# Optimization experiments

Measured on AMD Instinct MI355X. Metric: run time of the kernel, lower is better.

## Reference

```python
import jax, jax.numpy as jnp
from jax import lax
import numpy as np

EPS = 1e-5

def setup_inputs() -> dict:
    key = jax.random.key(0)
    k1, k2, k3, k4 = jax.random.split(key, 4)
    B, in_c, out_c, k, z_dim, H, W = 16, 128, 256, 3, 256, 64, 64
    fan_in = in_c * k * k
    x = jax.random.normal(k1, (B, in_c, H, W), dtype=jnp.float32)
    z = jax.random.normal(k2, (B, z_dim), dtype=jnp.float32)
    base_weight = jax.random.normal(k3, (out_c, in_c, k, k), dtype=jnp.float32) * np.sqrt(2.0 / fan_in)
    head_w = jax.random.normal(k4, (out_c * in_c * k * k, z_dim), dtype=jnp.float32) * np.sqrt(1.0 / z_dim)
    return {"x": x, "z": z, "base_weight": base_weight, "head_w": head_w}

def reference(x, z, base_weight, head_w):
    # x: [B, in_c, H, W]; z: [B, z_dim]; base_weight: [out_c, in_c, k, k]; head_w: [out_c*in_c*k*k, z_dim]
    B = x.shape[0]
    out_c, in_c, k, _ = base_weight.shape
    fan_in = in_c * k * k
    hyper_weight = 1.0

    # delta_w = Linear(z) -> [B, out_c, in_c, k, k]
    delta_w = jnp.einsum('bz,oz->bo', z, head_w).reshape(B, out_c, in_c, k, k)
    # standardize over (in_c, k, k) per (sample, out-channel)
    mu = jnp.mean(delta_w, axis=(2, 3, 4), keepdims=True)
    var = jnp.var(delta_w, axis=(2, 3, 4), keepdims=True)
    delta_w = (delta_w - mu) * lax.rsqrt(var + EPS)
    delta_w = delta_w * jnp.sqrt(2.0 / fan_in)

    w = (base_weight[None] + hyper_weight * delta_w) / jnp.sqrt(2.0)  # [B, out_c, in_c, k, k]

    pad = k // 2
    def conv_one(xb, wb):
        # xb: [in_c, H, W], wb: [out_c, in_c, k, k]
        return lax.conv_general_dilated(
            xb[None], wb, window_strides=(1, 1), padding=[(pad, pad), (pad, pad)],
            dimension_numbers=('NCHW', 'OIHW', 'NCHW'))[0]

    out = jax.vmap(conv_one)(x, w)  # [B, out_c, H_out, W_out]
    return out
```

## Files before the change

### kernel.cpp

```cpp
#include <hip/hip_runtime.h>

#define B_  16
#define IC  128
#define OC  256
#define ZD  256
#define HH  64
#define WW  64
#define FAN 1152
#define NO  294912
#define HP  66

typedef float    fvec4 __attribute__((ext_vector_type(4)));
typedef _Float16 f16x8 __attribute__((ext_vector_type(8)));
typedef _Float16 f16x4 __attribute__((ext_vector_type(4)));

__device__ __forceinline__ void gl_lds16(const _Float16* g, _Float16* ldst) {
  __builtin_amdgcn_global_load_lds(
      (const __attribute__((address_space(1))) unsigned int*)(const void*)g,
      (__attribute__((address_space(3))) unsigned int*)(void*)ldst,
      16, 0, 0);
}

#define BARRIER()  asm volatile("s_barrier" ::: "memory")
#define WAITLGKM() asm volatile("s_waitcnt lgkmcnt(0)" ::: "memory")

__global__ __launch_bounds__(512) void delta_std_fused_kernel(
    const float* __restrict__ z, const float* __restrict__ head_w,
    const float* __restrict__ base_w, _Float16* __restrict__ w_h) {
  __shared__ __align__(16) _Float16 As2[2][128 * 264];
  __shared__ _Float16 zsh[16 * 264];
  __shared__ float bsh[FAN];
  __shared__ float swS[8 * 16], swQ[8 * 16];
  __shared__ float musb[16], scb[16];

  const int t = threadIdx.x;
  const int oc = blockIdx.x;
  const int lane = t & 63, wave = t >> 6;
  const int quad = lane >> 4, l16 = lane & 15;

  const float* hw = head_w + (size_t)oc * FAN * ZD;
  const float* hwp = hw + (size_t)wave * ZD + lane * 4;

  fvec4 rg[16];
#pragma unroll
  for (int i = 0; i < 16; ++i)
    rg[i] = *(const fvec4*)(hwp + (size_t)i * 8 * ZD);

  for (int u = t; u < 1024; u += 512) {
    int b = u >> 6, kq = u & 63;
    fvec4 v = *(const fvec4*)&z[b * ZD + kq * 4];
    f16x4 h = {(_Float16)v.x, (_Float16)v.y, (_Float16)v.z, (_Float16)v.w};
    *(f16x4*)&zsh[b * 264 + kq * 4] = h;
  }
  for (int u = t; u < FAN; u += 512) bsh[u] = base_w[oc * FAN + u];

  fvec4 dd[9];

#pragma unroll
  for (int c = 0; c < 9; ++c) {
    _Float16* dst = &As2[c & 1][wave * 264 + lane * 4];
#pragma unroll
    for (int i = 0; i < 16; ++i) {
      fvec4 v = rg[i];
      f16x4 h = {(_Float16)v.x, (_Float16)v.y, (_Float16)v.z, (_Float16)v.w};
      *(f16x4*)(dst + i * 8 * 264) = h;
    }
    if (c < 8) {
      const float* src = hwp + (size_t)(c + 1) * 128 * ZD;
#pragma unroll
      for (int i = 0; i < 16; ++i)
        rg[i] = *(const fvec4*)(src + (size_t)i * 8 * ZD);
    }
    WAITLGKM();
    BARRIER();
    fvec4 a = (fvec4){0.f, 0.f, 0.f, 0.f};
    const _Float16* Ab = &As2[c & 1][(wave * 16 + l16) * 264 + quad * 8];
    const _Float16* Zb = &zsh[l16 * 264 + quad * 8];
#pragma unroll
    for (int kc = 0; kc < 8; ++kc) {
      f16x8 af = *(const f16x8*)(Ab + kc * 32);
      f16x8 bz = *(const f16x8*)(Zb + kc * 32);
      a = __builtin_amdgcn_mfma_f32_16x16x32_f16(af, bz, a, 0, 0, 0);
    }
    dd[c] = a;
    WAITLGKM();
    BARRIER();
  }

  float s = 0.f, s2 = 0.f;
#pragma unroll
  for (int c = 0; c < 9; ++c)
#pragma unroll
    for (int r = 0; r < 4; ++r) { float v = dd[c][r]; s += v; s2 += v * v; }
  s  += __shfl_xor(s, 16);  s  += __shfl_xor(s, 32);
  s2 += __shfl_xor(s2, 16); s2 += __shfl_xor(s2, 32);
  if (lane < 16) { swS[wave * 16 + l16] = s; swQ[wave * 16 + l16] = s2; }
  __syncthreads();
  if (t < 16) {
    float S = 0.f, S2 = 0.f;
#pragma unroll
    for (int w = 0; w < 8; ++w) { S += swS[w * 16 + t]; S2 += swQ[w * 16 + t]; }
    const float inv_fan = 1.0f / (float)FAN;
    float mu  = S * inv_fan;
    float var = S2 * inv_fan - mu * mu;
    const float inv_sqrt2 = 0.70710678118654752f;
    musb[t] = mu;
    scb[t]  = rsqrtf(var + 1e-5f) * sqrtf(2.0f / (float)FAN) * inv_sqrt2;
  }
  __syncthreads();

  float* dsh = (float*)&As2[0][0];
#pragma unroll
  for (int c = 0; c < 9; ++c) {
    int jb = c * 128 + wave * 16 + quad * 4;
#pragma unroll
    for (int r = 0; r < 4; ++r)
      dsh[(jb + r) * 17 + l16] = dd[c][r];
  }
  __syncthreads();

  const float inv_sqrt2 = 0.70710678118654752f;
  for (int u = t; u < 2304; u += 512) {
    int b = u / 144, seg = u % 144;
    int p0 = seg * 8;
    int kk = p0 >> 7, ic0 = p0 & 127;
    float mu = musb[b], sc = scb[b];
    _Float16 h[8];
#pragma unroll
    for (int e = 0; e < 8; ++e) {
      int j = (ic0 + e) * 9 + kk;
      float val = bsh[j] * inv_sqrt2 + (dsh[j * 17 + b] - mu) * sc;
      h[e] = (_Float16)val;
    }
    *(f16x8*)&w_h[((size_t)b * OC + oc) * FAN + p0] = *(f16x8*)h;
  }
}

__global__ __launch_bounds__(256) void xpose_kernel(
    const float* __restrict__ x, _Float16* __restrict__ x_h) {
  int yp = blockIdx.x;
  int b  = blockIdx.y;
  int t  = threadIdx.x;
  _Float16* orow = x_h + ((size_t)(b * HP + yp)) * HP * IC;

  if (yp == 0 || yp == HP - 1) {
    fvec4 zz = (fvec4){0.f, 0.f, 0.f, 0.f};
    for (int u = t; u < HP * IC / 8; u += 256)
      ((fvec4*)orow)[u] = zz;
    return;
  }
  int y = yp - 1;
  __shared__ float tile[128 * 65];
#pragma unroll
  for (int i = 0; i < 8; ++i) {
    int F = i * 256 + t;
    int ic = F >> 4, xq = F & 15;
    fvec4 v = *(const fvec4*)&x[(((size_t)b * IC + ic) * HH + y) * WW + xq * 4];
    float* tp = &tile[ic * 65 + xq * 4];
    tp[0] = v.x; tp[1] = v.y; tp[2] = v.z; tp[3] = v.w;
  }
  __syncthreads();
#pragma unroll
  for (int j = 0; j < 4; ++j) {
    int u = j * 256 + t;
    int px = u >> 4, icg = u & 15;
    _Float16 h[8];
#pragma unroll
    for (int c = 0; c < 8; ++c) h[c] = (_Float16)tile[(icg * 8 + c) * 65 + px];
    *(f16x8*)&orow[(px + 1) * IC + icg * 8] = *(f16x8*)h;
  }
  if (t < 32) {
    int side = t >> 4, icg = t & 15;
    fvec4 zz = (fvec4){0.f, 0.f, 0.f, 0.f};
    *(fvec4*)&orow[(side ? (HP - 1) * IC : 0) + icg * 8] = zz;
  }
}

__global__ __launch_bounds__(256) void conv_mfma_kernel(
    const _Float16* __restrict__ x_h, const _Float16* __restrict__ w_h,
    float* __restrict__ out) {
  __shared__ __align__(16) _Float16 As[128 * 64];
  __shared__ __align__(16) _Float16 Bs[128 * 64];
  int t = threadIdx.x;
  int b = blockIdx.z;
  int oc0 = blockIdx.y * 128;
  int y0 = blockIdx.x * 2;
  int lane = t & 63, wave = t >> 6;
  int wm = wave >> 1, wn = wave & 1;
  int quad = lane >> 4, l16 = lane & 15;

  fvec4 acc[4][4];
#pragma unroll
  for (int i = 0; i < 4; ++i)
#pragma unroll
    for (int j = 0; j < 4; ++j) acc[i][j] = (fvec4){0.f, 0.f, 0.f, 0.f};

  int lrow = lane >> 3;
  int lseg = lane & 7;
  int sw   = lseg ^ lrow;

  const _Float16* apg[4];
#pragma unroll
  for (int n = 0; n < 4; ++n)
    apg[n] = w_h + ((size_t)(b * OC + oc0 + wave * 32 + n * 8 + lrow)) * FAN + sw * 8;

  const _Float16* bpg0 =
      x_h + (((size_t)(b * HP + y0 + (wave >> 1))) * HP + (wave & 1) * 32 + lrow) * IC + sw * 8;
  const _Float16* bpg1 = bpg0 + 16 * IC;

  _Float16* adst = As + wave * 32 * 64;
  _Float16* bdst = Bs + wave * 32 * 64;

  int s7 = l16 & 7;
  int arow = (wm * 64 + l16) * 64;
  int brow = (wn * 64 + l16) * 64;
  int aoff[2] = { arow + ((0 + quad) ^ s7) * 8, arow + ((4 + quad) ^ s7) * 8 };
  int boff[2] = { brow + ((0 + quad) ^ s7) * 8, brow + ((4 + quad) ^ s7) * 8 };

#pragma unroll
  for (int ky = 0; ky < 3; ++ky) {
#pragma unroll
    for (int kx = 0; kx < 3; ++kx) {
      const int kk = ky * 3 + kx;
      const _Float16* b0k = bpg0 + (ky * HP + kx) * IC;
      const _Float16* b1k = bpg1 + (ky * HP + kx) * IC;
#pragma unroll
      for (int icc = 0; icc < 2; ++icc) {
        __syncthreads();
#pragma unroll
        for (int n = 0; n < 4; ++n)
          gl_lds16(apg[n] + kk * 128 + icc * 64, adst + n * 512);
        gl_lds16(b0k + icc * 64,        bdst);
        gl_lds16(b0k + 1024 + icc * 64, bdst + 512);
        gl_lds16(b1k + icc * 64,        bdst + 1024);
        gl_lds16(b1k + 1024 + icc * 64, bdst + 1536);
        __syncthreads();
#pragma unroll
        for (int ks = 0; ks < 2; ++ks) {
          f16x8 af[4], bf[4];
#pragma unroll
          for (int i = 0; i < 4; ++i)
            af[i] = *(const f16x8*)&As[aoff[ks] + i * 1024];
#pragma unroll
          for (int j = 0; j < 4; ++j)
            bf[j] = *(const f16x8*)&Bs[boff[ks] + j * 1024];
#pragma unroll
          for (int i = 0; i < 4; ++i)
#pragma unroll
            for (int j = 0; j < 4; ++j)
              acc[i][j] = __builtin_amdgcn_mfma_f32_16x16x32_f16(af[i], bf[j], acc[i][j], 0, 0, 0);
        }
      }
    }
  }

#pragma unroll
  for (int i = 0; i < 4; ++i)
#pragma unroll
    for (int j = 0; j < 4; ++j) {
      int m  = oc0 + wm * 64 + i * 16 + quad * 4;
      int nn = wn * 64 + j * 16 + l16;
      int oy = y0 + (nn >> 6), ox = nn & 63;
      float* op = out + (((size_t)(b * OC + m) * HH + oy) * WW + ox);
#pragma unroll
      for (int r = 0; r < 4; ++r)
        op[(size_t)r * HH * WW] = acc[i][j][r];
    }
}

extern "C" void kernel_launch(void* const* d_in, const int* in_sizes, int n_in,
                              void* d_out, int out_size, void* d_ws, size_t ws_size,
                              hipStream_t stream) {
  const float* x      = (const float*)d_in[0];
  const float* z      = (const float*)d_in[1];
  const float* base_w = (const float*)d_in[2];
  const float* head_w = (const float*)d_in[3];
  float* out = (float*)d_out;

  _Float16* w_h = (_Float16*)d_ws;
  _Float16* x_h = (_Float16*)((char*)d_ws + (size_t)B_ * OC * FAN * sizeof(_Float16));

  delta_std_fused_kernel<<<OC, 512, 0, stream>>>(z, head_w, base_w, w_h);
  xpose_kernel<<<dim3(HP, B_), 256, 0, stream>>>(x, x_h);
  conv_mfma_kernel<<<dim3(32, 2, B_), 256, 0, stream>>>(x_h, w_h, out);
}
```

Baseline: 487.6 us.

## Rewrite conv GEMM with 256x256 tiles and 4-stage async LDS pipeline

The conv kernel now uses 512-thread blocks that each compute all 256 output channels for 4 output rows, with each wave holding a 128x64 accumulator tile. Global-to-LDS loads go through a 4-slot ring buffer with vmcnt-based waits, so loads for later K-steps are in flight while MFMAs run, replacing the two-barrier load/compute pattern. It also adds an XOR swizzle for the 32-wide K segments and raises MFMA priority with setprio. The cost is more registers and LDS per block, fewer blocks in the grid, and fragile hand-written wait counts.

```diff
diff --git a/kernel.cpp b/kernel.cpp
--- a/kernel.cpp
+++ b/kernel.cpp
@@ -22,6 +22,9 @@
 }
 
 #define BARRIER()  asm volatile("s_barrier" ::: "memory")
+#define WAITVM8()  asm volatile("s_waitcnt vmcnt(8)" ::: "memory")
+#define WAITVM4()  asm volatile("s_waitcnt vmcnt(4)" ::: "memory")
+#define WAITVM0()  asm volatile("s_waitcnt vmcnt(0)" ::: "memory")
 #define WAITLGKM() asm volatile("s_waitcnt lgkmcnt(0)" ::: "memory")
 
 __global__ __launch_bounds__(512) void delta_std_fused_kernel(
@@ -176,95 +179,133 @@
   }
 }
 
-__global__ __launch_bounds__(256) void conv_mfma_kernel(
+__global__ __launch_bounds__(512, 2) void conv_mfma_kernel(
     const _Float16* __restrict__ x_h, const _Float16* __restrict__ w_h,
     float* __restrict__ out) {
-  __shared__ __align__(16) _Float16 As[128 * 64];
-  __shared__ __align__(16) _Float16 Bs[128 * 64];
-  int t = threadIdx.x;
-  int b = blockIdx.z;
-  int oc0 = blockIdx.y * 128;
-  int y0 = blockIdx.x * 2;
-  int lane = t & 63, wave = t >> 6;
-  int wm = wave >> 1, wn = wave & 1;
-  int quad = lane >> 4, l16 = lane & 15;
-
-  fvec4 acc[4][4];
-#pragma unroll
-  for (int i = 0; i < 4; ++i)
+  __shared__ __align__(16) _Float16 As[4 * 8192];
+  __shared__ __align__(16) _Float16 Bs[4 * 8192];
+  const int t = threadIdx.x;
+  const int b = blockIdx.y;
+  const int y0 = blockIdx.x * 4;
+  const int lane = t & 63, wave = t >> 6;
+  const int wm = wave >> 2, wn = wave & 3;
+  const int quad = lane >> 4, l16 = lane & 15;
+
+  fvec4 acc[8][4];
+#pragma unroll
+  for (int i = 0; i < 8; ++i)
 #pragma unroll
     for (int j = 0; j < 4; ++j) acc[i][j] = (fvec4){0.f, 0.f, 0.f, 0.f};
 
-  int lrow = lane >> 3;
-  int lseg = lane & 7;
-  int sw   = lseg ^ lrow;
-
-  const _Float16* apg[4];
-#pragma unroll
-  for (int n = 0; n < 4; ++n)
-    apg[n] = w_h + ((size_t)(b * OC + oc0 + wave * 32 + n * 8 + lrow)) * FAN + sw * 8;
-
+  const int lr = lane >> 2;
+  const int sw = (lane & 3) ^ (lr & 3) ^ ((lr >> 2) & 3);
+
+  const _Float16* apg0 = w_h + ((size_t)(b * OC + wave * 32 + lr)) * FAN + sw * 8;
+  const _Float16* apg1 = apg0 + (size_t)16 * FAN;
+  const int p0 = wave * 32 + lr, p1 = p0 + 16;
   const _Float16* bpg0 =
-      x_h + (((size_t)(b * HP + y0 + (wave >> 1))) * HP + (wave & 1) * 32 + lrow) * IC + sw * 8;
-  const _Float16* bpg1 = bpg0 + 16 * IC;
-
-  _Float16* adst = As + wave * 32 * 64;
-  _Float16* bdst = Bs + wave * 32 * 64;
-
-  int s7 = l16 & 7;
-  int arow = (wm * 64 + l16) * 64;
-  int brow = (wn * 64 + l16) * 64;
-  int aoff[2] = { arow + ((0 + quad) ^ s7) * 8, arow + ((4 + quad) ^ s7) * 8 };
-  int boff[2] = { brow + ((0 + quad) ^ s7) * 8, brow + ((4 + quad) ^ s7) * 8 };
-
-#pragma unroll
-  for (int ky = 0; ky < 3; ++ky) {
-#pragma unroll
-    for (int kx = 0; kx < 3; ++kx) {
-      const int kk = ky * 3 + kx;
-      const _Float16* b0k = bpg0 + (ky * HP + kx) * IC;
-      const _Float16* b1k = bpg1 + (ky * HP + kx) * IC;
-#pragma unroll
-      for (int icc = 0; icc < 2; ++icc) {
-        __syncthreads();
-#pragma unroll
-        for (int n = 0; n < 4; ++n)
-          gl_lds16(apg[n] + kk * 128 + icc * 64, adst + n * 512);
-        gl_lds16(b0k + icc * 64,        bdst);
-        gl_lds16(b0k + 1024 + icc * 64, bdst + 512);
-        gl_lds16(b1k + icc * 64,        bdst + 1024);
-        gl_lds16(b1k + 1024 + icc * 64, bdst + 1536);
-        __syncthreads();
-#pragma unroll
-        for (int ks = 0; ks < 2; ++ks) {
-          f16x8 af[4], bf[4];
-#pragma unroll
-          for (int i = 0; i < 4; ++i)
-            af[i] = *(const f16x8*)&As[aoff[ks] + i * 1024];
-#pragma unroll
-          for (int j = 0; j < 4; ++j)
-            bf[j] = *(const f16x8*)&Bs[boff[ks] + j * 1024];
-#pragma unroll
-          for (int i = 0; i < 4; ++i)
-#pragma unroll
-            for (int j = 0; j < 4; ++j)
-              acc[i][j] = __builtin_amdgcn_mfma_f32_16x16x32_f16(af[i], bf[j], acc[i][j], 0, 0, 0);
-        }
-      }
-    }
-  }
-
-#pragma unroll
-  for (int i = 0; i < 4; ++i)
-#pragma unroll
-    for (int j = 0; j < 4; ++j) {
-      int m  = oc0 + wm * 64 + i * 16 + quad * 4;
-      int nn = wn * 64 + j * 16 + l16;
-      int oy = y0 + (nn >> 6), ox = nn & 63;
-      float* op = out + (((size_t)(b * OC + m) * HH + oy) * WW + ox);
+      x_h + (((size_t)(b * HP + y0 + (p0 >> 6))) * HP + (p0 & 63)) * IC + sw * 8;
+  const _Float16* bpg1 =
+      x_h + (((size_t)(b * HP + y0 + (p1 >> 6))) * HP + (p1 & 63)) * IC + sw * 8;
+
+  const int dst0 = wave * 1024;
+
+  const int xoro = (l16 & 3) ^ ((l16 >> 2) & 3);
+  const int kseg = (quad ^ xoro) << 3;
+  const int arow = (wm * 128 + l16) * 32 + kseg;
+  const int brow = (wn * 64 + l16) * 32 + kseg;
+
+#define STAGE_A(KT, KS) do {                                        \
+    int sl_ = (((KT) * 2 + (KS)) & 3);                              \
+    int co_ = (KT) * 64 + (KS) * 32;                                \
+    gl_lds16(apg0 + co_, As + sl_ * 8192 + dst0);                   \
+    gl_lds16(apg1 + co_, As + sl_ * 8192 + dst0 + 512);             \
+  } while (0)
+#define STAGE_B(KT, KS) do {                                        \
+    int sl_ = (((KT) * 2 + (KS)) & 3);                              \
+    int tap_ = (KT) >> 1;                                           \
+    int ky_ = (tap_ * 11) >> 5;                                     \
+    int kx_ = tap_ - ky_ * 3;                                       \
+    int co_ = (ky_ * HP + kx_) * IC + ((KT) & 1) * 64 + (KS) * 32;  \
+    gl_lds16(bpg0 + co_, Bs + sl_ * 8192 + dst0);                   \
+    gl_lds16(bpg1 + co_, Bs + sl_ * 8192 + dst0 + 512);             \
+  } while (0)
+#define MFMA16(H)                                                   \
+    __builtin_amdgcn_s_setprio(1);                                  \
+    _Pragma("unroll")                                               \
+    for (int mf = 0; mf < 8; ++mf) {                                \
+      acc[mf][(H)*2]   = __builtin_amdgcn_mfma_f32_16x16x32_f16(af[mf], bf0, acc[mf][(H)*2],   0, 0, 0); \
+      acc[mf][(H)*2+1] = __builtin_amdgcn_mfma_f32_16x16x32_f16(af[mf], bf1, acc[mf][(H)*2+1], 0, 0, 0); \
+    }                                                               \
+    __builtin_amdgcn_s_setprio(0);
+
+#define KT_BODY(KT, S01, S23, VM1, VM3) {                           \
+    const int sA0 = (((KT) * 2) & 3) * 8192;                        \
+    const int sA1 = (((KT) * 2 + 1) & 3) * 8192;                    \
+    f16x8 af[8], bf0, bf1;                                          \
+                                         \
+    _Pragma("unroll")                                               \
+    for (int mf = 0; mf < 8; ++mf)                                  \
+      af[mf] = *(const f16x8*)&As[sA0 + arow + mf * 512];           \
+    bf0 = *(const f16x8*)&Bs[sA0 + brow];                           \
+    bf1 = *(const f16x8*)&Bs[sA0 + brow + 512];                     \
+    if (S01) STAGE_A((KT) + 1, 1);                                  \
+    WAITVM8(); BARRIER();                                           \
+    MFMA16(0);                                                      \
+    BARRIER();                                                      \
+                                         \
+    bf0 = *(const f16x8*)&Bs[sA0 + brow + 1024];                    \
+    bf1 = *(const f16x8*)&Bs[sA0 + brow + 1536];                    \
+    if (S01) STAGE_B((KT) + 1, 1);                                  \
+    VM1; BARRIER();                                                 \
+    MFMA16(1);                                                      \
+    BARRIER();                                                      \
+                                         \
+    _Pragma("unroll")                                               \
+    for (int mf = 0; mf < 8; ++mf)                                  \
+      af[mf] = *(const f16x8*)&As[sA1 + arow + mf * 512];           \
+    bf0 = *(const f16x8*)&Bs[sA1 + brow];                           \
+    bf1 = *(const f16x8*)&Bs[sA1 + brow + 512];                     \
+    if (S23) STAGE_A((KT) + 2, 0);                                  \
+    WAITVM8(); BARRIER();                                           \
+    MFMA16(0);                                                      \
+    BARRIER();                                                      \
+                                         \
+    bf0 = *(const f16x8*)&Bs[sA1 + brow + 1024];                    \
+    bf1 = *(const f16x8*)&Bs[sA1 + brow + 1536];                    \
+    if (S23) STAGE_B((KT) + 2, 0);                                  \
+    VM3; BARRIER();                                                 \
+    MFMA16(1);                                                      \
+    BARRIER();                                                      \
+  }
+
+  STAGE_A(0, 0); STAGE_B(0, 0);
+  STAGE_A(0, 1); STAGE_B(0, 1);
+  STAGE_A(1, 0); STAGE_B(1, 0);
+  WAITVM8(); BARRIER();
+
+#pragma unroll 1
+  for (int kt = 0; kt < 16; ++kt)
+    KT_BODY(kt, 1, 1, WAITVM8(), WAITVM8());
+  KT_BODY(16, 1, 0, WAITVM8(), WAITVM4());
+  KT_BODY(17, 0, 0, WAITVM0(), (void)0);
+
+#undef KT_BODY
+#undef MFMA16
+#undef STAGE_B
+#undef STAGE_A
+
+#pragma unroll
+  for (int mf = 0; mf < 8; ++mf)
+#pragma unroll
+    for (int nf = 0; nf < 4; ++nf) {
+      int oc = wm * 128 + mf * 16 + quad * 4;
+      int pn = wn * 64 + nf * 16 + l16;
+      int oy = y0 + (pn >> 6), ox = pn & 63;
+      float* op = out + (((size_t)(b * OC + oc) * HH + oy) * WW + ox);
 #pragma unroll
       for (int r = 0; r < 4; ++r)
-        op[(size_t)r * HH * WW] = acc[i][j][r];
+        op[(size_t)r * HH * WW] = acc[mf][nf][r];
     }
 }
 
@@ -282,5 +323,5 @@
 
   delta_std_fused_kernel<<<OC, 512, 0, stream>>>(z, head_w, base_w, w_h);
   xpose_kernel<<<dim3(HP, B_), 256, 0, stream>>>(x, x_h);
-  conv_mfma_kernel<<<dim3(32, 2, B_), 256, 0, stream>>>(x_h, w_h, out);
-}
+  conv_mfma_kernel<<<dim3(16, B_), 512, 0, stream>>>(x_h, w_h, out);
+}
```

New measurement: 490.5 us. Within noise of the previous version (+0.6%).
